# Kernel tuning notes

Hardware: AMD Instinct MI355X
Metric: run time of the kernel (lower is better)

Reference implementation:

```python
import jax, jax.numpy as jnp
import numpy as np

SC, ST, B, D, H, E, F, TOPK = 2048, 2048, 4, 256, 4, 8, 1024, 2
AUXW = 0.01
EPS = 1e-5


def setup_inputs() -> dict:
    key = jax.random.key(0)
    ks = jax.random.split(key, 16)
    s = 0.02
    n = lambda k, shp: (jax.random.normal(k, shp, jnp.float32) * s)
    z = lambda shp: jnp.zeros(shp, jnp.float32)
    o = lambda shp: jnp.ones(shp, jnp.float32)
    return {
        "x_context": jax.random.normal(ks[0], (SC, B, D), jnp.float32),
        "x_target": jax.random.normal(ks[1], (ST, B, D), jnp.float32),
        # shared self/cross attention (separate_att=False)
        "Wq": n(ks[2], (D, D)), "Wk": n(ks[3], (D, D)), "Wv": n(ks[4], (D, D)),
        "bq": z(D), "bk": z(D), "bv": z(D),
        "Wo": n(ks[5], (D, D)), "bo": z(D),
        # MoE gating + stacked 2-layer expert MLPs (D -> F -> D)
        "Wg": n(ks[6], (D, E)), "bg": z(E),
        "W1": n(ks[7], (E, D, F)), "b1": z((E, F)),
        "W2": n(ks[8], (E, F, D)), "b2": z((E, D)),
        # four post-LayerNorms
        "g_c1": o(D), "b_c1": z(D), "g_c2": o(D), "b_c2": z(D),
        "g_t1": o(D), "b_t1": z(D), "g_t2": o(D), "b_t2": z(D),
    }


def _ln(x, g, b):
    mu = x.mean(-1, keepdims=True)
    var = ((x - mu) ** 2).mean(-1, keepdims=True)
    return (x - mu) * jax.lax.rsqrt(var + EPS) * g + b


def _mha(q_in, kv, Wq, Wk, Wv, bq, bk, bv, Wo, bo):
    Sq, Bt, Dm = q_in.shape
    Sk = kv.shape[0]
    dh = Dm // H
    q = (q_in @ Wq + bq).reshape(Sq, Bt, H, dh)
    k = (kv @ Wk + bk).reshape(Sk, Bt, H, dh)
    v = (kv @ Wv + bv).reshape(Sk, Bt, H, dh)
    scores = jnp.einsum('qbhd,kbhd->bhqk', q, k) / jnp.asarray(np.sqrt(dh), q.dtype)
    attn = jax.nn.softmax(scores, axis=-1)
    out = jnp.einsum('bhqk,kbhd->qbhd', attn, v).reshape(Sq, Bt, Dm)
    return out @ Wo + bo


def _moe(x, Wg, bg, W1, b1, W2, b2):
    shp = x.shape
    xf = x.reshape(-1, shp[-1])          # [T, D]
    T = xf.shape[0]
    probs = jax.nn.softmax(xf @ Wg + bg, axis=-1)   # [T, E]
    gv, gi = jax.lax.top_k(probs, TOPK)
    gv = gv / gv.sum(-1, keepdims=True)
    # dense combine weights: gate value if expert selected else 0
    comb = jnp.zeros((T, E), xf.dtype).at[jnp.arange(T)[:, None], gi].add(gv)
    out = jnp.zeros_like(xf)
    for e in range(E):                    # fixed small expert loop
        h = jax.nn.relu(xf @ W1[e] + b1[e])
        out = out + (h @ W2[e] + b2[e]) * comb[:, e:e + 1]
    counts = probs.sum(0)
    frac = counts / counts.sum()
    aux = E * jnp.sum(frac * probs.mean(0))
    return out.reshape(shp), aux


def reference(x_context, x_target, Wq, Wk, Wv, bq, bk, bv, Wo, bo,
              Wg, bg, W1, b1, W2, b2,
              g_c1, b_c1, g_c2, b_c2, g_t1, b_t1, g_t2, b_t2):
    # context self-attention (post-norm)
    a = _mha(x_context, x_context, Wq, Wk, Wv, bq, bk, bv, Wo, bo)
    xc = _ln(a + x_context, g_c1, b_c1)
    f, aux1 = _moe(xc, Wg, bg, W1, b1, W2, b2)
    xc = _ln(f + xc, g_c2, b_c2)
    # target cross-attention over context (shared attention weights)
    a = _mha(x_target, xc, Wq, Wk, Wv, bq, bk, bv, Wo, bo)
    xt = _ln(a + x_target, g_t1, b_t1)
    f, aux2 = _moe(xt, Wg, bg, W1, b1, W2, b2)
    xt = _ln(f + xt, g_t2, b_t2)
    aux = AUXW * (aux1 + aux2)
    return xc, xt, aux
```

## Files before the change

kernel.cpp:

```cpp
#include <hip/hip_runtime.h>
#include <hip/hip_bf16.h>

typedef _Float16 f16_t;
typedef _Float16 f16x4v __attribute__((ext_vector_type(4)));
typedef _Float16 f16x8 __attribute__((ext_vector_type(8)));
typedef float f32x4 __attribute__((ext_vector_type(4)));

template<bool BIAS, bool OUTF16>
__global__ __launch_bounds__(256) void gemm16_kernel(
    const f16_t* __restrict__ A, const f16_t* __restrict__ B, void* __restrict__ Cv,
    const float* __restrict__ bias, int M, int N, int K, int lda, int ldb, int ldc)
{
    __shared__ f16_t As[64][72];
    __shared__ f16_t Bs[64][72];
    const int m0 = blockIdx.y * 64, n0 = blockIdx.x * 64;
    const int t = threadIdx.x, wave = t >> 6, lane = t & 63;
    const int wr = (wave >> 1) * 32, wc = (wave & 1) * 32;
    const int lr = lane & 15, kg = lane >> 4;
    const int sr = t >> 2, sc = (t & 3) * 16;
    const f16_t* arp = A + (long long)(m0 + sr) * lda;
    const f16_t* brp = B + (long long)(n0 + sr) * ldb;

    f32x4 acc[2][2] = {};
    for (int k0 = 0; k0 < K; k0 += 64) {
        *reinterpret_cast<f16x8*>(&As[sr][sc])     = *reinterpret_cast<const f16x8*>(&arp[k0 + sc]);
        *reinterpret_cast<f16x8*>(&As[sr][sc + 8]) = *reinterpret_cast<const f16x8*>(&arp[k0 + sc + 8]);
        *reinterpret_cast<f16x8*>(&Bs[sr][sc])     = *reinterpret_cast<const f16x8*>(&brp[k0 + sc]);
        *reinterpret_cast<f16x8*>(&Bs[sr][sc + 8]) = *reinterpret_cast<const f16x8*>(&brp[k0 + sc + 8]);
        __syncthreads();
        #pragma unroll
        for (int c = 0; c < 2; c++) {
            f16x8 a0 = *reinterpret_cast<const f16x8*>(&As[wr + lr][c * 32 + kg * 8]);
            f16x8 a1 = *reinterpret_cast<const f16x8*>(&As[wr + 16 + lr][c * 32 + kg * 8]);
            f16x8 b0 = *reinterpret_cast<const f16x8*>(&Bs[wc + lr][c * 32 + kg * 8]);
            f16x8 b1 = *reinterpret_cast<const f16x8*>(&Bs[wc + 16 + lr][c * 32 + kg * 8]);
            acc[0][0] = __builtin_amdgcn_mfma_f32_16x16x32_f16(a0, b0, acc[0][0], 0, 0, 0);
            acc[0][1] = __builtin_amdgcn_mfma_f32_16x16x32_f16(a0, b1, acc[0][1], 0, 0, 0);
            acc[1][0] = __builtin_amdgcn_mfma_f32_16x16x32_f16(a1, b0, acc[1][0], 0, 0, 0);
            acc[1][1] = __builtin_amdgcn_mfma_f32_16x16x32_f16(a1, b1, acc[1][1], 0, 0, 0);
        }
        __syncthreads();
    }
    #pragma unroll
    for (int mi = 0; mi < 2; mi++)
        #pragma unroll
        for (int ni = 0; ni < 2; ni++)
            #pragma unroll
            for (int r = 0; r < 4; r++) {
                const int row = m0 + wr + mi * 16 + kg * 4 + r;
                const int col = n0 + wc + ni * 16 + lr;
                float v = acc[mi][ni][r];
                if constexpr (BIAS) v += bias[col];
                if constexpr (OUTF16) ((f16_t*)Cv)[(long long)row * ldc + col] = (f16_t)v;
                else                  ((float*)Cv)[(long long)row * ldc + col] = v;
            }
}

__global__ __launch_bounds__(256) void qkv_kernel(
    const f16_t* __restrict__ Aq, const f16_t* __restrict__ Akv,
    const f16_t* __restrict__ B0, const f16_t* __restrict__ B1, const f16_t* __restrict__ B2,
    const float* __restrict__ bi0, const float* __restrict__ bi1, const float* __restrict__ bi2,
    f16_t* __restrict__ C0, f16_t* __restrict__ C1, f16_t* __restrict__ C2)
{
    const int zz = blockIdx.z;
    const f16_t* A = (zz == 0) ? Aq : Akv;
    const f16_t* B = (zz == 0) ? B0 : (zz == 1 ? B1 : B2);
    const float* bias = (zz == 0) ? bi0 : (zz == 1 ? bi1 : bi2);
    f16_t* C = (zz == 0) ? C0 : (zz == 1 ? C1 : C2);

    __shared__ f16_t As[64][72];
    __shared__ f16_t Bs[64][72];
    const int m0 = blockIdx.y * 64, n0 = blockIdx.x * 64;
    const int t = threadIdx.x, wave = t >> 6, lane = t & 63;
    const int wr = (wave >> 1) * 32, wc = (wave & 1) * 32;
    const int lr = lane & 15, kg = lane >> 4;
    const int sr = t >> 2, sc = (t & 3) * 16;
    const f16_t* arp = A + (long long)(m0 + sr) * 256;
    const f16_t* brp = B + (long long)(n0 + sr) * 256;

    f32x4 acc[2][2] = {};
    for (int k0 = 0; k0 < 256; k0 += 64) {
        *reinterpret_cast<f16x8*>(&As[sr][sc])     = *reinterpret_cast<const f16x8*>(&arp[k0 + sc]);
        *reinterpret_cast<f16x8*>(&As[sr][sc + 8]) = *reinterpret_cast<const f16x8*>(&arp[k0 + sc + 8]);
        *reinterpret_cast<f16x8*>(&Bs[sr][sc])     = *reinterpret_cast<const f16x8*>(&brp[k0 + sc]);
        *reinterpret_cast<f16x8*>(&Bs[sr][sc + 8]) = *reinterpret_cast<const f16x8*>(&brp[k0 + sc + 8]);
        __syncthreads();
        #pragma unroll
        for (int c = 0; c < 2; c++) {
            f16x8 a0 = *reinterpret_cast<const f16x8*>(&As[wr + lr][c * 32 + kg * 8]);
            f16x8 a1 = *reinterpret_cast<const f16x8*>(&As[wr + 16 + lr][c * 32 + kg * 8]);
            f16x8 b0 = *reinterpret_cast<const f16x8*>(&Bs[wc + lr][c * 32 + kg * 8]);
            f16x8 b1 = *reinterpret_cast<const f16x8*>(&Bs[wc + 16 + lr][c * 32 + kg * 8]);
            acc[0][0] = __builtin_amdgcn_mfma_f32_16x16x32_f16(a0, b0, acc[0][0], 0, 0, 0);
            acc[0][1] = __builtin_amdgcn_mfma_f32_16x16x32_f16(a0, b1, acc[0][1], 0, 0, 0);
            acc[1][0] = __builtin_amdgcn_mfma_f32_16x16x32_f16(a1, b0, acc[1][0], 0, 0, 0);
            acc[1][1] = __builtin_amdgcn_mfma_f32_16x16x32_f16(a1, b1, acc[1][1], 0, 0, 0);
        }
        __syncthreads();
    }
    #pragma unroll
    for (int mi = 0; mi < 2; mi++)
        #pragma unroll
        for (int ni = 0; ni < 2; ni++)
            #pragma unroll
            for (int r = 0; r < 4; r++) {
                const int row = m0 + wr + mi * 16 + kg * 4 + r;
                const int col = n0 + wc + ni * 16 + lr;
                C[(long long)row * 256 + col] = (f16_t)(acc[mi][ni][r] + bias[col]);
            }
}

template<bool GATHER, bool RELU, bool OUTF16>
__global__ __launch_bounds__(256) void moe_gemm16_kernel(
    const f16_t* __restrict__ A, const int* __restrict__ tok_of_slot,
    const f16_t* __restrict__ W, const float* __restrict__ bias,
    void* __restrict__ Cv, const int* __restrict__ ebase,
    int N, int K, int lda, int ldb, int ldc, int wstride, int bstride)
{
    const int m0 = blockIdx.y * 64;
    if (m0 >= ebase[8]) return;
    int e = 0;
    #pragma unroll
    for (int i = 1; i < 8; i++) if (m0 >= ebase[i]) e = i;
    const f16_t* __restrict__ B = W + (long long)e * wstride;
    const float* __restrict__ bs = bias + e * bstride;

    __shared__ f16_t As[64][72];
    __shared__ f16_t Bs[64][72];
    const int n0 = blockIdx.x * 64;
    const int t = threadIdx.x, wave = t >> 6, lane = t & 63;
    const int wr = (wave >> 1) * 32, wc = (wave & 1) * 32;
    const int lr = lane & 15, kg = lane >> 4;
    const int sr = t >> 2, sc = (t & 3) * 16;
    const f16_t* arp;
    if constexpr (GATHER) arp = A + (long long)(tok_of_slot[m0 + sr] & 8191) * lda;
    else                  arp = A + (long long)(m0 + sr) * lda;
    const f16_t* brp = B + (long long)(n0 + sr) * ldb;

    f32x4 acc[2][2] = {};
    for (int k0 = 0; k0 < K; k0 += 64) {
        *reinterpret_cast<f16x8*>(&As[sr][sc])     = *reinterpret_cast<const f16x8*>(&arp[k0 + sc]);
        *reinterpret_cast<f16x8*>(&As[sr][sc + 8]) = *reinterpret_cast<const f16x8*>(&arp[k0 + sc + 8]);
        *reinterpret_cast<f16x8*>(&Bs[sr][sc])     = *reinterpret_cast<const f16x8*>(&brp[k0 + sc]);
        *reinterpret_cast<f16x8*>(&Bs[sr][sc + 8]) = *reinterpret_cast<const f16x8*>(&brp[k0 + sc + 8]);
        __syncthreads();
        #pragma unroll
        for (int c = 0; c < 2; c++) {
            f16x8 a0 = *reinterpret_cast<const f16x8*>(&As[wr + lr][c * 32 + kg * 8]);
            f16x8 a1 = *reinterpret_cast<const f16x8*>(&As[wr + 16 + lr][c * 32 + kg * 8]);
            f16x8 b0 = *reinterpret_cast<const f16x8*>(&Bs[wc + lr][c * 32 + kg * 8]);
            f16x8 b1 = *reinterpret_cast<const f16x8*>(&Bs[wc + 16 + lr][c * 32 + kg * 8]);
            acc[0][0] = __builtin_amdgcn_mfma_f32_16x16x32_f16(a0, b0, acc[0][0], 0, 0, 0);
            acc[0][1] = __builtin_amdgcn_mfma_f32_16x16x32_f16(a0, b1, acc[0][1], 0, 0, 0);
            acc[1][0] = __builtin_amdgcn_mfma_f32_16x16x32_f16(a1, b0, acc[1][0], 0, 0, 0);
            acc[1][1] = __builtin_amdgcn_mfma_f32_16x16x32_f16(a1, b1, acc[1][1], 0, 0, 0);
        }
        __syncthreads();
    }
    #pragma unroll
    for (int mi = 0; mi < 2; mi++)
        #pragma unroll
        for (int ni = 0; ni < 2; ni++)
            #pragma unroll
            for (int r = 0; r < 4; r++) {
                const int row = m0 + wr + mi * 16 + kg * 4 + r;
                const int col = n0 + wc + ni * 16 + lr;
                float v = acc[mi][ni][r] + bs[col];
                if constexpr (RELU) v = fmaxf(v, 0.f);
                if constexpr (OUTF16) ((f16_t*)Cv)[(long long)row * ldc + col] = (f16_t)v;
                else                  ((float*)Cv)[(long long)row * ldc + col] = v;
            }
}

__global__ __launch_bounds__(256) void vtrans_kernel(
    const f16_t* __restrict__ V16, f16_t* __restrict__ VT)
{
    __shared__ f16_t tile[32][33];
    const int z = blockIdx.z;
    const int s0 = blockIdx.x * 32, d0 = blockIdx.y * 32;
    const int tx = threadIdx.x & 31, ty = threadIdx.x >> 5;
    #pragma unroll
    for (int i = 0; i < 32; i += 8)
        tile[ty + i][tx] = V16[(long long)(s0 + ty + i) * 1024 + 64 * z + d0 + tx];
    __syncthreads();
    #pragma unroll
    for (int i = 0; i < 32; i += 8)
        VT[(long long)z * 131072 + (long long)(d0 + ty + i) * 2048 + s0 + tx] = tile[tx][ty + i];
}

__global__ __launch_bounds__(256, 6) void flash_kernel(
    const f16_t* __restrict__ Q16, const f16_t* __restrict__ K16,
    const f16_t* __restrict__ VT, f16_t* __restrict__ Opart,
    float* __restrict__ mlm, float* __restrict__ mll)
{
    __shared__ f16_t KVs[64][72];
    __shared__ f16_t Ps[4][16][72];

    const int z = blockIdx.y;
    const int c = blockIdx.z;
    const int m0 = blockIdx.x * 64;
    const int t = threadIdx.x, w = t >> 6, lane = t & 63;
    const int lr = lane & 15, kg = lane >> 4;
    const long long cbase = 64LL * z;

    f16x8 qf0, qf1;
    {
        const long long qrow = (long long)(m0 + w * 16 + lr) * 1024 + cbase;
        qf0 = *reinterpret_cast<const f16x8*>(&Q16[qrow + kg * 8]);
        qf1 = *reinterpret_cast<const f16x8*>(&Q16[qrow + 32 + kg * 8]);
        #pragma unroll
        for (int i = 0; i < 8; i++) { qf0[i] *= (f16_t)0.125f; qf1[i] *= (f16_t)0.125f; }
    }

    f32x4 oacc[4] = {};
    float mrun[4] = { -1e30f, -1e30f, -1e30f, -1e30f };
    float lrun[4] = {};

    const int sr = t >> 2, sc = (t & 3) * 16;
    const int nbeg = c * 512;
    for (int n0 = nbeg; n0 < nbeg + 512; n0 += 64) {
        const long long krow = (long long)(n0 + sr) * 1024 + cbase;
        *reinterpret_cast<f16x8*>(&KVs[sr][sc])     = *reinterpret_cast<const f16x8*>(&K16[krow + sc]);
        *reinterpret_cast<f16x8*>(&KVs[sr][sc + 8]) = *reinterpret_cast<const f16x8*>(&K16[krow + sc + 8]);
        __syncthreads();

        float sv[4][4];
        #pragma unroll
        for (int nt = 0; nt < 4; nt++) {
            f32x4 acc = {};
            f16x8 b0 = *reinterpret_cast<const f16x8*>(&KVs[nt * 16 + lr][kg * 8]);
            f16x8 b1 = *reinterpret_cast<const f16x8*>(&KVs[nt * 16 + lr][32 + kg * 8]);
            acc = __builtin_amdgcn_mfma_f32_16x16x32_f16(qf0, b0, acc, 0, 0, 0);
            acc = __builtin_amdgcn_mfma_f32_16x16x32_f16(qf1, b1, acc, 0, 0, 0);
            #pragma unroll
            for (int r = 0; r < 4; r++) sv[nt][r] = acc[r];
        }

        float mnew[4], alpha[4];
        #pragma unroll
        for (int r = 0; r < 4; r++) {
            float rm = fmaxf(fmaxf(sv[0][r], sv[1][r]), fmaxf(sv[2][r], sv[3][r]));
            rm = fmaxf(rm, __shfl_xor(rm, 1));
            rm = fmaxf(rm, __shfl_xor(rm, 2));
            rm = fmaxf(rm, __shfl_xor(rm, 4));
            rm = fmaxf(rm, __shfl_xor(rm, 8));
            mnew[r] = fmaxf(mrun[r], rm);
            alpha[r] = __expf(mrun[r] - mnew[r]);
            mrun[r] = mnew[r];
        }
        #pragma unroll
        for (int nt = 0; nt < 4; nt++)
            #pragma unroll
            for (int r = 0; r < 4; r++) sv[nt][r] = __expf(sv[nt][r] - mnew[r]);
        #pragma unroll
        for (int r = 0; r < 4; r++) {
            float rs = sv[0][r] + sv[1][r] + sv[2][r] + sv[3][r];
            rs += __shfl_xor(rs, 1);
            rs += __shfl_xor(rs, 2);
            rs += __shfl_xor(rs, 4);
            rs += __shfl_xor(rs, 8);
            lrun[r] = lrun[r] * alpha[r] + rs;
        }
        #pragma unroll
        for (int dt = 0; dt < 4; dt++)
            #pragma unroll
            for (int r = 0; r < 4; r++) oacc[dt][r] *= alpha[r];

        #pragma unroll
        for (int nt = 0; nt < 4; nt++)
            #pragma unroll
            for (int r = 0; r < 4; r++)
                Ps[w][kg * 4 + r][nt * 16 + lr] = (f16_t)sv[nt][r];

        __syncthreads();

        const long long vrow = (long long)z * 131072 + (long long)sr * 2048 + n0;
        *reinterpret_cast<f16x8*>(&KVs[sr][sc])     = *reinterpret_cast<const f16x8*>(&VT[vrow + sc]);
        *reinterpret_cast<f16x8*>(&KVs[sr][sc + 8]) = *reinterpret_cast<const f16x8*>(&VT[vrow + sc + 8]);
        __syncthreads();

        f16x8 pa0 = *reinterpret_cast<const f16x8*>(&Ps[w][lr][kg * 8]);
        f16x8 pa1 = *reinterpret_cast<const f16x8*>(&Ps[w][lr][32 + kg * 8]);
        #pragma unroll
        for (int dt = 0; dt < 4; dt++) {
            f16x8 vb0 = *reinterpret_cast<const f16x8*>(&KVs[dt * 16 + lr][kg * 8]);
            f16x8 vb1 = *reinterpret_cast<const f16x8*>(&KVs[dt * 16 + lr][32 + kg * 8]);
            oacc[dt] = __builtin_amdgcn_mfma_f32_16x16x32_f16(pa0, vb0, oacc[dt], 0, 0, 0);
            oacc[dt] = __builtin_amdgcn_mfma_f32_16x16x32_f16(pa1, vb1, oacc[dt], 0, 0, 0);
        }
        __syncthreads();
    }

    f16_t* op = Opart + (long long)c * 2097152;
    const long long orow0 = (long long)(m0 + w * 16) * 1024 + cbase;
    #pragma unroll
    for (int r = 0; r < 4; r++)
        #pragma unroll
        for (int dt = 0; dt < 4; dt++)
            op[orow0 + (long long)(kg * 4 + r) * 1024 + dt * 16 + lr] = (f16_t)oacc[dt][r];
    if (lr == 0) {
        const int b = z >> 2, h = z & 3;
        #pragma unroll
        for (int r = 0; r < 4; r++) {
            const int tok = (m0 + w * 16 + kg * 4 + r) * 4 + b;
            const long long idx = (long long)(c * 4 + h) * 8192 + tok;
            mlm[idx] = mrun[r];
            mll[idx] = lrun[r];
        }
    }
}

__global__ __launch_bounds__(256) void merge_kernel(
    const f16_t* __restrict__ Opart, const float* __restrict__ mlm,
    const float* __restrict__ mll, f16_t* __restrict__ O16)
{
    const int w = threadIdx.x >> 6, lane = threadIdx.x & 63;
    const int trow = blockIdx.x * 4 + w;
    const int h = lane >> 4;
    float m[4], l[4];
    #pragma unroll
    for (int c = 0; c < 4; c++) {
        m[c] = mlm[(long long)(c * 4 + h) * 8192 + trow];
        l[c] = mll[(long long)(c * 4 + h) * 8192 + trow];
    }
    float M = fmaxf(fmaxf(m[0], m[1]), fmaxf(m[2], m[3]));
    float wv[4], L = 0.f;
    #pragma unroll
    for (int c = 0; c < 4; c++) { wv[c] = __expf(m[c] - M); L += wv[c] * l[c]; }
    const float inv = 1.f / L;
    const long long base = (long long)trow * 256 + lane * 4;
    float acc[4] = {};
    #pragma unroll
    for (int c = 0; c < 4; c++) {
        f16x4v v = *reinterpret_cast<const f16x4v*>(&Opart[(long long)c * 2097152 + base]);
        #pragma unroll
        for (int j = 0; j < 4; j++) acc[j] += wv[c] * (float)v[j];
    }
    f16_t o[4] = { (f16_t)(acc[0] * inv), (f16_t)(acc[1] * inv),
                   (f16_t)(acc[2] * inv), (f16_t)(acc[3] * inv) };
    *reinterpret_cast<ulong1*>(&O16[base]) = *reinterpret_cast<ulong1*>(o);
}

__global__ __launch_bounds__(256) void wtrans_kernel(
    const float* __restrict__ in, f16_t* __restrict__ out, int R, int C)
{
    __shared__ float tile[32][33];
    const long long zoff = (long long)blockIdx.z * R * C;
    const int r0 = blockIdx.y * 32, c0 = blockIdx.x * 32;
    const int tx = threadIdx.x & 31, ty = threadIdx.x >> 5;
    #pragma unroll
    for (int i = 0; i < 32; i += 8)
        tile[ty + i][tx] = in[zoff + (long long)(r0 + ty + i) * C + c0 + tx];
    __syncthreads();
    #pragma unroll
    for (int i = 0; i < 32; i += 8)
        out[zoff + (long long)(c0 + ty + i) * R + r0 + tx] = (f16_t)tile[tx][ty + i];
}

__global__ __launch_bounds__(256) void wtrans4_kernel(
    const float* __restrict__ W0, const float* __restrict__ W1,
    const float* __restrict__ W2, const float* __restrict__ W3,
    f16_t* __restrict__ T0, f16_t* __restrict__ T1,
    f16_t* __restrict__ T2, f16_t* __restrict__ T3)
{
    __shared__ float tile[32][33];
    const int z = blockIdx.z;
    const float* in = (z == 0) ? W0 : (z == 1 ? W1 : (z == 2 ? W2 : W3));
    f16_t* out = (z == 0) ? T0 : (z == 1 ? T1 : (z == 2 ? T2 : T3));
    const int r0 = blockIdx.y * 32, c0 = blockIdx.x * 32;
    const int tx = threadIdx.x & 31, ty = threadIdx.x >> 5;
    #pragma unroll
    for (int i = 0; i < 32; i += 8)
        tile[ty + i][tx] = in[(long long)(r0 + ty + i) * 256 + c0 + tx];
    __syncthreads();
    #pragma unroll
    for (int i = 0; i < 32; i += 8)
        out[(long long)(c0 + ty + i) * 256 + r0 + tx] = (f16_t)tile[tx][ty + i];
}

__global__ __launch_bounds__(256) void cvt16_kernel(
    const float* __restrict__ a, const float* __restrict__ b,
    f16_t* __restrict__ oa, f16_t* __restrict__ ob)
{
    long long i = ((long long)blockIdx.x * 256 + threadIdx.x) * 4;
    const float* in = a; f16_t* out = oa;
    if (i >= 2097152) { in = b; out = ob; i -= 2097152; }
    float4 v = *reinterpret_cast<const float4*>(&in[i]);
    f16_t o[4] = { (f16_t)v.x, (f16_t)v.y, (f16_t)v.z, (f16_t)v.w };
    *reinterpret_cast<ulong1*>(&out[i]) = *reinterpret_cast<ulong1*>(o);
}

__global__ __launch_bounds__(256) void ln_kernel(
    const float* __restrict__ in1, const float* __restrict__ in2,
    const float* __restrict__ gamma, const float* __restrict__ beta,
    float* __restrict__ out, f16_t* __restrict__ out16)
{
    const int wave = threadIdx.x >> 6, lane = threadIdx.x & 63;
    const long long row = (long long)blockIdx.x * 4 + wave;
    const long long base = row * 256 + lane * 4;
    float4 a = *reinterpret_cast<const float4*>(&in1[base]);
    float4 b = *reinterpret_cast<const float4*>(&in2[base]);
    float x[4] = { a.x + b.x, a.y + b.y, a.z + b.z, a.w + b.w };
    float s = x[0] + x[1] + x[2] + x[3];
    float s2 = x[0]*x[0] + x[1]*x[1] + x[2]*x[2] + x[3]*x[3];
    #pragma unroll
    for (int o = 32; o; o >>= 1) { s += __shfl_xor(s, o); s2 += __shfl_xor(s2, o); }
    const float mean = s * (1.f / 256.f);
    const float var = s2 * (1.f / 256.f) - mean * mean;
    const float rstd = rsqrtf(var + 1e-5f);
    float4 g = *reinterpret_cast<const float4*>(&gamma[lane * 4]);
    float4 bb = *reinterpret_cast<const float4*>(&beta[lane * 4]);
    const float* gf = reinterpret_cast<const float*>(&g);
    const float* bf = reinterpret_cast<const float*>(&bb);
    float y[4];
    #pragma unroll
    for (int i = 0; i < 4; i++) y[i] = (x[i] - mean) * rstd * gf[i] + bf[i];
    *reinterpret_cast<float4*>(&out[base]) = make_float4(y[0], y[1], y[2], y[3]);
    if (out16) {
        f16_t o[4] = { (f16_t)y[0], (f16_t)y[1], (f16_t)y[2], (f16_t)y[3] };
        *reinterpret_cast<ulong1*>(&out16[base]) = *reinterpret_cast<ulong1*>(o);
    }
}

__global__ __launch_bounds__(256) void gating_kernel(
    const float* __restrict__ X, const float* __restrict__ Wg, const float* __restrict__ bg,
    int* __restrict__ gcount, float* __restrict__ counts,
    int* __restrict__ pos_of_tok, int* __restrict__ exp_of_tok,
    float* __restrict__ gate_of_tok)
{
    __shared__ float WgL[2048];
    __shared__ float cpart[8];
    __shared__ int lcnt[8];
    __shared__ int lbase[8];
    const int t = threadIdx.x;
    for (int i = t; i < 2048; i += 256) WgL[i] = Wg[i];
    if (t < 8) { cpart[t] = 0.f; lcnt[t] = 0; }
    __syncthreads();

    const int tok = blockIdx.x * 256 + t;
    const float* xr = X + (long long)tok * 256;
    float acc[8] = {};
    for (int k = 0; k < 256; k += 4) {
        float4 xv = *reinterpret_cast<const float4*>(xr + k);
        const float* xf = reinterpret_cast<const float*>(&xv);
        #pragma unroll
        for (int i = 0; i < 4; i++) {
            const float xi = xf[i];
            const float* wrow = &WgL[(k + i) * 8];
            #pragma unroll
            for (int e = 0; e < 8; e++) acc[e] += xi * wrow[e];
        }
    }
    float p[8]; float mx = -1e30f;
    #pragma unroll
    for (int e = 0; e < 8; e++) { p[e] = acc[e] + bg[e]; mx = fmaxf(mx, p[e]); }
    float se = 0.f;
    #pragma unroll
    for (int e = 0; e < 8; e++) { p[e] = __expf(p[e] - mx); se += p[e]; }
    const float inv = 1.f / se;
    #pragma unroll
    for (int e = 0; e < 8; e++) { p[e] *= inv; atomicAdd(&cpart[e], p[e]); }

    int i1 = 0;
    #pragma unroll
    for (int e = 1; e < 8; e++) if (p[e] > p[i1]) i1 = e;
    int i2 = (i1 == 0) ? 1 : 0;
    #pragma unroll
    for (int e = 0; e < 8; e++) if (e != i1 && p[e] > p[i2]) i2 = e;
    const float gs = 1.f / (p[i1] + p[i2]);

    const int p1 = atomicAdd(&lcnt[i1], 1);
    const int p2 = atomicAdd(&lcnt[i2], 1);
    __syncthreads();
    if (t < 8) {
        lbase[t] = atomicAdd(&gcount[t], lcnt[t]);
        atomicAdd(&counts[t], cpart[t]);
    }
    __syncthreads();
    pos_of_tok[2 * tok]     = lbase[i1] + p1;
    pos_of_tok[2 * tok + 1] = lbase[i2] + p2;
    exp_of_tok[2 * tok]     = i1;
    exp_of_tok[2 * tok + 1] = i2;
    gate_of_tok[2 * tok]     = p[i1] * gs;
    gate_of_tok[2 * tok + 1] = p[i2] * gs;
}

__global__ void finalize_kernel(const int* __restrict__ gcount, int* __restrict__ ebase)
{
    if (threadIdx.x == 0) {
        int b = 0;
        for (int e = 0; e < 8; e++) { ebase[e] = b; b += (gcount[e] + 63) & ~63; }
        ebase[8] = b;
    }
}

__global__ __launch_bounds__(256) void scatter_kernel(
    const int* __restrict__ pos_of_tok, const int* __restrict__ exp_of_tok,
    const int* __restrict__ ebase, int* __restrict__ tok_of_slot)
{
    const int i = blockIdx.x * 256 + threadIdx.x;
    const int e = exp_of_tok[i];
    tok_of_slot[ebase[e] + pos_of_tok[i]] = i >> 1;
}

__global__ __launch_bounds__(256) void moe_combine_ln_kernel(
    const float* __restrict__ Ys, const float* __restrict__ X1,
    const int* __restrict__ pos_of_tok, const int* __restrict__ exp_of_tok,
    const float* __restrict__ gate_of_tok, const int* __restrict__ ebase,
    const float* __restrict__ gamma, const float* __restrict__ beta,
    float* __restrict__ out, f16_t* __restrict__ out16)
{
    const int wave = threadIdx.x >> 6, lane = threadIdx.x & 63;
    const long long tok = (long long)blockIdx.x * 4 + wave;
    const int e1 = exp_of_tok[2 * tok], e2 = exp_of_tok[2 * tok + 1];
    const long long s1 = ebase[e1] + pos_of_tok[2 * tok];
    const long long s2 = ebase[e2] + pos_of_tok[2 * tok + 1];
    const float gv1 = gate_of_tok[2 * tok], gv2 = gate_of_tok[2 * tok + 1];
    const long long base = tok * 256 + lane * 4;
    float4 y1 = *reinterpret_cast<const float4*>(&Ys[s1 * 256 + lane * 4]);
    float4 y2 = *reinterpret_cast<const float4*>(&Ys[s2 * 256 + lane * 4]);
    float4 xv = *reinterpret_cast<const float4*>(&X1[base]);
    float x[4] = { gv1 * y1.x + gv2 * y2.x + xv.x,
                   gv1 * y1.y + gv2 * y2.y + xv.y,
                   gv1 * y1.z + gv2 * y2.z + xv.z,
                   gv1 * y1.w + gv2 * y2.w + xv.w };
    float s = x[0] + x[1] + x[2] + x[3];
    float s2v = x[0]*x[0] + x[1]*x[1] + x[2]*x[2] + x[3]*x[3];
    #pragma unroll
    for (int o = 32; o; o >>= 1) { s += __shfl_xor(s, o); s2v += __shfl_xor(s2v, o); }
    const float mean = s * (1.f / 256.f);
    const float var = s2v * (1.f / 256.f) - mean * mean;
    const float rstd = rsqrtf(var + 1e-5f);
    float4 g = *reinterpret_cast<const float4*>(&gamma[lane * 4]);
    float4 bb = *reinterpret_cast<const float4*>(&beta[lane * 4]);
    const float* gf = reinterpret_cast<const float*>(&g);
    const float* bf = reinterpret_cast<const float*>(&bb);
    float y[4];
    #pragma unroll
    for (int i = 0; i < 4; i++) y[i] = (x[i] - mean) * rstd * gf[i] + bf[i];
    *reinterpret_cast<float4*>(&out[base]) = make_float4(y[0], y[1], y[2], y[3]);
    if (out16) {
        f16_t o[4] = { (f16_t)y[0], (f16_t)y[1], (f16_t)y[2], (f16_t)y[3] };
        *reinterpret_cast<ulong1*>(&out16[base]) = *reinterpret_cast<ulong1*>(o);
    }
}

__global__ void aux_kernel(const float* __restrict__ counts, float* __restrict__ out)
{
    if (threadIdx.x == 0) {
        float aux = 0.f;
        for (int pzz = 0; pzz < 2; pzz++) {
            const float* c = counts + pzz * 8;
            float tot = 0.f;
            for (int e = 0; e < 8; e++) tot += c[e];
            float s = 0.f;
            for (int e = 0; e < 8; e++) s += (c[e] / tot) * (c[e] * (1.f / 8192.f));
            aux += 8.f * s;
        }
        out[0] = 0.01f * aux;
    }
}

extern "C" void kernel_launch(void* const* d_in, const int* in_sizes, int n_in,
                              void* d_out, int out_size, void* d_ws, size_t ws_size,
                              hipStream_t stream)
{
    const float* Xc  = (const float*)d_in[0];
    const float* Xt  = (const float*)d_in[1];
    const float* Wq  = (const float*)d_in[2];
    const float* Wk  = (const float*)d_in[3];
    const float* Wv  = (const float*)d_in[4];
    const float* bq  = (const float*)d_in[5];
    const float* bk  = (const float*)d_in[6];
    const float* bv  = (const float*)d_in[7];
    const float* Wo  = (const float*)d_in[8];
    const float* bo  = (const float*)d_in[9];
    const float* Wg  = (const float*)d_in[10];
    const float* bg  = (const float*)d_in[11];
    const float* W1  = (const float*)d_in[12];
    const float* b1  = (const float*)d_in[13];
    const float* W2  = (const float*)d_in[14];
    const float* b2  = (const float*)d_in[15];
    const float* g_c1 = (const float*)d_in[16];
    const float* b_c1 = (const float*)d_in[17];
    const float* g_c2 = (const float*)d_in[18];
    const float* b_c2 = (const float*)d_in[19];
    const float* g_t1 = (const float*)d_in[20];
    const float* b_t1 = (const float*)d_in[21];
    const float* g_t2 = (const float*)d_in[22];
    const float* b_t2 = (const float*)d_in[23];

    const long long NTOK = 2097152;
    const int SLOT_MAX = 16896;
    float* dout = (float*)d_out;
    float* xcout = dout;
    float* xtout = dout + NTOK;

    float* ws = (float*)d_ws;
    float* P1 = ws;
    float* X1 = P1 + NTOK;
    float* Ys = X1 + NTOK;
    float* counts      = Ys + (long long)SLOT_MAX * 256;
    int*   gcount      = (int*)(counts + 16);
    float* gate_of_tok = (float*)(gcount + 16);
    float* mlm = gate_of_tok + 16384;
    float* mll = mlm + 131072;
    int* ebase       = (int*)(mll + 131072);
    int* pos_of_tok  = ebase + 16;
    int* exp_of_tok  = pos_of_tok + 16384;
    int* tok_of_slot = exp_of_tok + 16384;
    f16_t* h16 = (f16_t*)(tok_of_slot + SLOT_MAX);
    f16_t* Xc16 = h16;
    f16_t* Xt16 = Xc16 + NTOK;
    f16_t* xc16 = Xt16 + NTOK;
    f16_t* Q16  = xc16 + NTOK;
    f16_t* K16  = Q16 + NTOK;
    f16_t* V16  = K16 + NTOK;
    f16_t* O16  = V16 + NTOK;
    f16_t* X116 = O16 + NTOK;
    f16_t* VT   = X116 + NTOK;
    f16_t* Hs16 = VT + NTOK;
    f16_t* WqT  = Hs16 + (long long)SLOT_MAX * 1024;
    f16_t* WkT  = WqT + 65536;
    f16_t* WvT  = WkT + 65536;
    f16_t* WoT  = WvT + 65536;
    f16_t* W1T  = WoT + 65536;
    f16_t* W2T  = W1T + 2097152;
    f16_t* Opart = Hs16;

    hipMemsetAsync(counts, 0, 32 * sizeof(int), stream);

    cvt16_kernel<<<4096, 256, 0, stream>>>(Xc, Xt, Xc16, Xt16);
    wtrans4_kernel<<<dim3(8, 8, 4), 256, 0, stream>>>(Wq, Wk, Wv, Wo, WqT, WkT, WvT, WoT);
    wtrans_kernel<<<dim3(32, 8, 8), 256, 0, stream>>>(W1, W1T, 256, 1024);
    wtrans_kernel<<<dim3(8, 32, 8), 256, 0, stream>>>(W2, W2T, 1024, 256);

    for (int pass = 0; pass < 2; pass++) {
        const float*  xq    = pass ? Xt   : Xc;
        const f16_t*  xq16  = pass ? Xt16 : Xc16;
        const f16_t*  xkv16 = pass ? xc16 : Xc16;
        const float* g1  = pass ? g_t1 : g_c1;
        const float* be1 = pass ? b_t1 : b_c1;
        const float* g2  = pass ? g_t2 : g_c2;
        const float* be2 = pass ? b_t2 : b_c2;
        float* cnt = counts + pass * 8;
        int* gcnt  = gcount + pass * 8;
        float* oln = pass ? xtout : xcout;
        f16_t* oln16 = pass ? nullptr : xc16;

        qkv_kernel<<<dim3(4, 128, 3), 256, 0, stream>>>(
            xq16, xkv16, WqT, WkT, WvT, bq, bk, bv, Q16, K16, V16);

        vtrans_kernel<<<dim3(64, 2, 16), 256, 0, stream>>>(V16, VT);
        flash_kernel<<<dim3(32, 16, 4), 256, 0, stream>>>(Q16, K16, VT, Opart, mlm, mll);
        merge_kernel<<<2048, 256, 0, stream>>>(Opart, mlm, mll, O16);

        gemm16_kernel<true,false><<<dim3(4, 128), 256, 0, stream>>>(
            O16, WoT, P1, bo, 8192, 256, 256, 256, 256, 256);
        ln_kernel<<<2048, 256, 0, stream>>>(P1, xq, g1, be1, X1, X116);

        gating_kernel<<<32, 256, 0, stream>>>(X1, Wg, bg, gcnt, cnt,
                                              pos_of_tok, exp_of_tok, gate_of_tok);
        finalize_kernel<<<1, 64, 0, stream>>>(gcnt, ebase);
        scatter_kernel<<<64, 256, 0, stream>>>(pos_of_tok, exp_of_tok, ebase, tok_of_slot);
        moe_gemm16_kernel<true,true,true><<<dim3(16, 264), 256, 0, stream>>>(
            X116, tok_of_slot, W1T, b1, Hs16, ebase,
            1024, 256, 256, 256, 1024, 262144, 1024);
        moe_gemm16_kernel<false,false,false><<<dim3(4, 264), 256, 0, stream>>>(
            Hs16, nullptr, W2T, b2, Ys, ebase,
            256, 1024, 1024, 1024, 256, 262144, 256);
        moe_combine_ln_kernel<<<2048, 256, 0, stream>>>(
            Ys, X1, pos_of_tok, exp_of_tok, gate_of_tok, ebase, g2, be2, oln, oln16);
    }

    aux_kernel<<<1, 64, 0, stream>>>(counts, dout + 2 * NTOK);
}
```

Baseline: 580.9 us.

## Use 128x128 GEMM tiles, prefetch K/V in flash, store MoE output as fp16

All GEMMs (QKV, output projection, both MoE expert GEMMs) now go through one shared body that computes 128x128 tiles, each wave holding a 4x4 set of MFMA accumulators. Expert padding is changed to 128 rows to match. The aim is more reuse of data staged in shared memory and fewer global loads per FLOP, at the cost of more registers, lower occupancy, fewer blocks and more padding waste. The flash kernel now loads the next K/V tile into registers before computing on the current one, and the second MoE GEMM writes fp16 instead of fp32, halving that traffic at some precision cost.

```diff
diff --git a/kernel.cpp b/kernel.cpp
--- a/kernel.cpp
+++ b/kernel.cpp
@@ -6,57 +6,77 @@
 typedef _Float16 f16x8 __attribute__((ext_vector_type(8)));
 typedef float f32x4 __attribute__((ext_vector_type(4)));
 
-template<bool BIAS, bool OUTF16>
-__global__ __launch_bounds__(256) void gemm16_kernel(
-    const f16_t* __restrict__ A, const f16_t* __restrict__ B, void* __restrict__ Cv,
-    const float* __restrict__ bias, int M, int N, int K, int lda, int ldb, int ldc)
-{
-    __shared__ f16_t As[64][72];
-    __shared__ f16_t Bs[64][72];
-    const int m0 = blockIdx.y * 64, n0 = blockIdx.x * 64;
+template<bool BIAS, bool RELU, bool OUTF16, bool GATHER>
+__device__ __forceinline__ void gemm128_body(
+    const f16_t* __restrict__ A, const f16_t* __restrict__ B,
+    void* __restrict__ Cv, const float* __restrict__ bias,
+    const int* __restrict__ tok_of_slot,
+    int m0, int n0, int K, int lda, int ldb, int ldc)
+{
+    __shared__ f16_t As[128][72];
+    __shared__ f16_t Bs[128][72];
     const int t = threadIdx.x, wave = t >> 6, lane = t & 63;
-    const int wr = (wave >> 1) * 32, wc = (wave & 1) * 32;
+    const int wr2 = (wave >> 1) * 64, wc2 = (wave & 1) * 64;
     const int lr = lane & 15, kg = lane >> 4;
-    const int sr = t >> 2, sc = (t & 3) * 16;
-    const f16_t* arp = A + (long long)(m0 + sr) * lda;
+    const int sr = t >> 1, sc0 = (t & 1) * 32;
+
+    const f16_t* arp;
+    if constexpr (GATHER) arp = A + (long long)(tok_of_slot[m0 + sr] & 8191) * lda;
+    else                  arp = A + (long long)(m0 + sr) * lda;
     const f16_t* brp = B + (long long)(n0 + sr) * ldb;
 
-    f32x4 acc[2][2] = {};
+    f32x4 acc[4][4] = {};
     for (int k0 = 0; k0 < K; k0 += 64) {
-        *reinterpret_cast<f16x8*>(&As[sr][sc])     = *reinterpret_cast<const f16x8*>(&arp[k0 + sc]);
-        *reinterpret_cast<f16x8*>(&As[sr][sc + 8]) = *reinterpret_cast<const f16x8*>(&arp[k0 + sc + 8]);
-        *reinterpret_cast<f16x8*>(&Bs[sr][sc])     = *reinterpret_cast<const f16x8*>(&brp[k0 + sc]);
-        *reinterpret_cast<f16x8*>(&Bs[sr][sc + 8]) = *reinterpret_cast<const f16x8*>(&brp[k0 + sc + 8]);
+        #pragma unroll
+        for (int j = 0; j < 4; j++) {
+            *reinterpret_cast<f16x8*>(&As[sr][sc0 + j * 8]) =
+                *reinterpret_cast<const f16x8*>(&arp[k0 + sc0 + j * 8]);
+            *reinterpret_cast<f16x8*>(&Bs[sr][sc0 + j * 8]) =
+                *reinterpret_cast<const f16x8*>(&brp[k0 + sc0 + j * 8]);
+        }
         __syncthreads();
         #pragma unroll
         for (int c = 0; c < 2; c++) {
-            f16x8 a0 = *reinterpret_cast<const f16x8*>(&As[wr + lr][c * 32 + kg * 8]);
-            f16x8 a1 = *reinterpret_cast<const f16x8*>(&As[wr + 16 + lr][c * 32 + kg * 8]);
-            f16x8 b0 = *reinterpret_cast<const f16x8*>(&Bs[wc + lr][c * 32 + kg * 8]);
-            f16x8 b1 = *reinterpret_cast<const f16x8*>(&Bs[wc + 16 + lr][c * 32 + kg * 8]);
-            acc[0][0] = __builtin_amdgcn_mfma_f32_16x16x32_f16(a0, b0, acc[0][0], 0, 0, 0);
-            acc[0][1] = __builtin_amdgcn_mfma_f32_16x16x32_f16(a0, b1, acc[0][1], 0, 0, 0);
-            acc[1][0] = __builtin_amdgcn_mfma_f32_16x16x32_f16(a1, b0, acc[1][0], 0, 0, 0);
-            acc[1][1] = __builtin_amdgcn_mfma_f32_16x16x32_f16(a1, b1, acc[1][1], 0, 0, 0);
+            f16x8 av[4], bv[4];
+            #pragma unroll
+            for (int i = 0; i < 4; i++) {
+                av[i] = *reinterpret_cast<const f16x8*>(&As[wr2 + i * 16 + lr][c * 32 + kg * 8]);
+                bv[i] = *reinterpret_cast<const f16x8*>(&Bs[wc2 + i * 16 + lr][c * 32 + kg * 8]);
+            }
+            #pragma unroll
+            for (int mi = 0; mi < 4; mi++)
+                #pragma unroll
+                for (int ni = 0; ni < 4; ni++)
+                    acc[mi][ni] = __builtin_amdgcn_mfma_f32_16x16x32_f16(av[mi], bv[ni], acc[mi][ni], 0, 0, 0);
         }
         __syncthreads();
     }
     #pragma unroll
-    for (int mi = 0; mi < 2; mi++)
-        #pragma unroll
-        for (int ni = 0; ni < 2; ni++)
+    for (int mi = 0; mi < 4; mi++)
+        #pragma unroll
+        for (int ni = 0; ni < 4; ni++)
             #pragma unroll
             for (int r = 0; r < 4; r++) {
-                const int row = m0 + wr + mi * 16 + kg * 4 + r;
-                const int col = n0 + wc + ni * 16 + lr;
+                const int row = m0 + wr2 + mi * 16 + kg * 4 + r;
+                const int col = n0 + wc2 + ni * 16 + lr;
                 float v = acc[mi][ni][r];
                 if constexpr (BIAS) v += bias[col];
+                if constexpr (RELU) v = fmaxf(v, 0.f);
                 if constexpr (OUTF16) ((f16_t*)Cv)[(long long)row * ldc + col] = (f16_t)v;
                 else                  ((float*)Cv)[(long long)row * ldc + col] = v;
             }
 }
 
-__global__ __launch_bounds__(256) void qkv_kernel(
+template<bool BIAS, bool OUTF16>
+__global__ __launch_bounds__(256) void gemm128_kernel(
+    const f16_t* __restrict__ A, const f16_t* __restrict__ B, void* __restrict__ Cv,
+    const float* __restrict__ bias, int K, int lda, int ldb, int ldc)
+{
+    gemm128_body<BIAS, false, OUTF16, false>(A, B, Cv, bias, nullptr,
+                                             blockIdx.y * 128, blockIdx.x * 128, K, lda, ldb, ldc);
+}
+
+__global__ __launch_bounds__(256) void qkv128_kernel(
     const f16_t* __restrict__ Aq, const f16_t* __restrict__ Akv,
     const f16_t* __restrict__ B0, const f16_t* __restrict__ B1, const f16_t* __restrict__ B2,
     const float* __restrict__ bi0, const float* __restrict__ bi1, const float* __restrict__ bi2,
@@ -67,109 +87,25 @@
     const f16_t* B = (zz == 0) ? B0 : (zz == 1 ? B1 : B2);
     const float* bias = (zz == 0) ? bi0 : (zz == 1 ? bi1 : bi2);
     f16_t* C = (zz == 0) ? C0 : (zz == 1 ? C1 : C2);
-
-    __shared__ f16_t As[64][72];
-    __shared__ f16_t Bs[64][72];
-    const int m0 = blockIdx.y * 64, n0 = blockIdx.x * 64;
-    const int t = threadIdx.x, wave = t >> 6, lane = t & 63;
-    const int wr = (wave >> 1) * 32, wc = (wave & 1) * 32;
-    const int lr = lane & 15, kg = lane >> 4;
-    const int sr = t >> 2, sc = (t & 3) * 16;
-    const f16_t* arp = A + (long long)(m0 + sr) * 256;
-    const f16_t* brp = B + (long long)(n0 + sr) * 256;
-
-    f32x4 acc[2][2] = {};
-    for (int k0 = 0; k0 < 256; k0 += 64) {
-        *reinterpret_cast<f16x8*>(&As[sr][sc])     = *reinterpret_cast<const f16x8*>(&arp[k0 + sc]);
-        *reinterpret_cast<f16x8*>(&As[sr][sc + 8]) = *reinterpret_cast<const f16x8*>(&arp[k0 + sc + 8]);
-        *reinterpret_cast<f16x8*>(&Bs[sr][sc])     = *reinterpret_cast<const f16x8*>(&brp[k0 + sc]);
-        *reinterpret_cast<f16x8*>(&Bs[sr][sc + 8]) = *reinterpret_cast<const f16x8*>(&brp[k0 + sc + 8]);
-        __syncthreads();
-        #pragma unroll
-        for (int c = 0; c < 2; c++) {
-            f16x8 a0 = *reinterpret_cast<const f16x8*>(&As[wr + lr][c * 32 + kg * 8]);
-            f16x8 a1 = *reinterpret_cast<const f16x8*>(&As[wr + 16 + lr][c * 32 + kg * 8]);
-            f16x8 b0 = *reinterpret_cast<const f16x8*>(&Bs[wc + lr][c * 32 + kg * 8]);
-            f16x8 b1 = *reinterpret_cast<const f16x8*>(&Bs[wc + 16 + lr][c * 32 + kg * 8]);
-            acc[0][0] = __builtin_amdgcn_mfma_f32_16x16x32_f16(a0, b0, acc[0][0], 0, 0, 0);
-            acc[0][1] = __builtin_amdgcn_mfma_f32_16x16x32_f16(a0, b1, acc[0][1], 0, 0, 0);
-            acc[1][0] = __builtin_amdgcn_mfma_f32_16x16x32_f16(a1, b0, acc[1][0], 0, 0, 0);
-            acc[1][1] = __builtin_amdgcn_mfma_f32_16x16x32_f16(a1, b1, acc[1][1], 0, 0, 0);
-        }
-        __syncthreads();
-    }
-    #pragma unroll
-    for (int mi = 0; mi < 2; mi++)
-        #pragma unroll
-        for (int ni = 0; ni < 2; ni++)
-            #pragma unroll
-            for (int r = 0; r < 4; r++) {
-                const int row = m0 + wr + mi * 16 + kg * 4 + r;
-                const int col = n0 + wc + ni * 16 + lr;
-                C[(long long)row * 256 + col] = (f16_t)(acc[mi][ni][r] + bias[col]);
-            }
-}
-
-template<bool GATHER, bool RELU, bool OUTF16>
-__global__ __launch_bounds__(256) void moe_gemm16_kernel(
+    gemm128_body<true, false, true, false>(A, B, C, bias, nullptr,
+                                           blockIdx.y * 128, blockIdx.x * 128, 256, 256, 256, 256);
+}
+
+template<bool RELU, bool OUTF16, bool GATHER>
+__global__ __launch_bounds__(256) void moe_gemm128_kernel(
     const f16_t* __restrict__ A, const int* __restrict__ tok_of_slot,
     const f16_t* __restrict__ W, const float* __restrict__ bias,
     void* __restrict__ Cv, const int* __restrict__ ebase,
-    int N, int K, int lda, int ldb, int ldc, int wstride, int bstride)
-{
-    const int m0 = blockIdx.y * 64;
+    int K, int lda, int ldb, int ldc, int wstride, int bstride)
+{
+    const int m0 = blockIdx.y * 128;
     if (m0 >= ebase[8]) return;
     int e = 0;
     #pragma unroll
     for (int i = 1; i < 8; i++) if (m0 >= ebase[i]) e = i;
-    const f16_t* __restrict__ B = W + (long long)e * wstride;
-    const float* __restrict__ bs = bias + e * bstride;
-
-    __shared__ f16_t As[64][72];
-    __shared__ f16_t Bs[64][72];
-    const int n0 = blockIdx.x * 64;
-    const int t = threadIdx.x, wave = t >> 6, lane = t & 63;
-    const int wr = (wave >> 1) * 32, wc = (wave & 1) * 32;
-    const int lr = lane & 15, kg = lane >> 4;
-    const int sr = t >> 2, sc = (t & 3) * 16;
-    const f16_t* arp;
-    if constexpr (GATHER) arp = A + (long long)(tok_of_slot[m0 + sr] & 8191) * lda;
-    else                  arp = A + (long long)(m0 + sr) * lda;
-    const f16_t* brp = B + (long long)(n0 + sr) * ldb;
-
-    f32x4 acc[2][2] = {};
-    for (int k0 = 0; k0 < K; k0 += 64) {
-        *reinterpret_cast<f16x8*>(&As[sr][sc])     = *reinterpret_cast<const f16x8*>(&arp[k0 + sc]);
-        *reinterpret_cast<f16x8*>(&As[sr][sc + 8]) = *reinterpret_cast<const f16x8*>(&arp[k0 + sc + 8]);
-        *reinterpret_cast<f16x8*>(&Bs[sr][sc])     = *reinterpret_cast<const f16x8*>(&brp[k0 + sc]);
-        *reinterpret_cast<f16x8*>(&Bs[sr][sc + 8]) = *reinterpret_cast<const f16x8*>(&brp[k0 + sc + 8]);
-        __syncthreads();
-        #pragma unroll
-        for (int c = 0; c < 2; c++) {
-            f16x8 a0 = *reinterpret_cast<const f16x8*>(&As[wr + lr][c * 32 + kg * 8]);
-            f16x8 a1 = *reinterpret_cast<const f16x8*>(&As[wr + 16 + lr][c * 32 + kg * 8]);
-            f16x8 b0 = *reinterpret_cast<const f16x8*>(&Bs[wc + lr][c * 32 + kg * 8]);
-            f16x8 b1 = *reinterpret_cast<const f16x8*>(&Bs[wc + 16 + lr][c * 32 + kg * 8]);
-            acc[0][0] = __builtin_amdgcn_mfma_f32_16x16x32_f16(a0, b0, acc[0][0], 0, 0, 0);
-            acc[0][1] = __builtin_amdgcn_mfma_f32_16x16x32_f16(a0, b1, acc[0][1], 0, 0, 0);
-            acc[1][0] = __builtin_amdgcn_mfma_f32_16x16x32_f16(a1, b0, acc[1][0], 0, 0, 0);
-            acc[1][1] = __builtin_amdgcn_mfma_f32_16x16x32_f16(a1, b1, acc[1][1], 0, 0, 0);
-        }
-        __syncthreads();
-    }
-    #pragma unroll
-    for (int mi = 0; mi < 2; mi++)
-        #pragma unroll
-        for (int ni = 0; ni < 2; ni++)
-            #pragma unroll
-            for (int r = 0; r < 4; r++) {
-                const int row = m0 + wr + mi * 16 + kg * 4 + r;
-                const int col = n0 + wc + ni * 16 + lr;
-                float v = acc[mi][ni][r] + bs[col];
-                if constexpr (RELU) v = fmaxf(v, 0.f);
-                if constexpr (OUTF16) ((f16_t*)Cv)[(long long)row * ldc + col] = (f16_t)v;
-                else                  ((float*)Cv)[(long long)row * ldc + col] = v;
-            }
+    gemm128_body<true, RELU, OUTF16, GATHER>(
+        A, W + (long long)e * wstride, Cv, bias + e * bstride, tok_of_slot,
+        m0, blockIdx.x * 128, K, lda, ldb, ldc);
 }
 
 __global__ __launch_bounds__(256) void vtrans_kernel(
@@ -217,12 +153,27 @@
     float lrun[4] = {};
 
     const int sr = t >> 2, sc = (t & 3) * 16;
-    const int nbeg = c * 512;
-    for (int n0 = nbeg; n0 < nbeg + 512; n0 += 64) {
-        const long long krow = (long long)(n0 + sr) * 1024 + cbase;
-        *reinterpret_cast<f16x8*>(&KVs[sr][sc])     = *reinterpret_cast<const f16x8*>(&K16[krow + sc]);
-        *reinterpret_cast<f16x8*>(&KVs[sr][sc + 8]) = *reinterpret_cast<const f16x8*>(&K16[krow + sc + 8]);
+    const int nbeg = c * 512, nend = nbeg + 512;
+
+    f16x8 ka, kb, va, vb;
+    {
+        const long long krow = (long long)(nbeg + sr) * 1024 + cbase;
+        ka = *reinterpret_cast<const f16x8*>(&K16[krow + sc]);
+        kb = *reinterpret_cast<const f16x8*>(&K16[krow + sc + 8]);
+        const long long vrow = (long long)z * 131072 + (long long)sr * 2048 + nbeg;
+        va = *reinterpret_cast<const f16x8*>(&VT[vrow + sc]);
+        vb = *reinterpret_cast<const f16x8*>(&VT[vrow + sc + 8]);
+    }
+
+    for (int n0 = nbeg; n0 < nend; n0 += 64) {
+        *reinterpret_cast<f16x8*>(&KVs[sr][sc])     = ka;
+        *reinterpret_cast<f16x8*>(&KVs[sr][sc + 8]) = kb;
         __syncthreads();
+        if (n0 + 64 < nend) {
+            const long long krow = (long long)(n0 + 64 + sr) * 1024 + cbase;
+            ka = *reinterpret_cast<const f16x8*>(&K16[krow + sc]);
+            kb = *reinterpret_cast<const f16x8*>(&K16[krow + sc + 8]);
+        }
 
         float sv[4][4];
         #pragma unroll
@@ -274,10 +225,14 @@
 
         __syncthreads();
 
-        const long long vrow = (long long)z * 131072 + (long long)sr * 2048 + n0;
-        *reinterpret_cast<f16x8*>(&KVs[sr][sc])     = *reinterpret_cast<const f16x8*>(&VT[vrow + sc]);
-        *reinterpret_cast<f16x8*>(&KVs[sr][sc + 8]) = *reinterpret_cast<const f16x8*>(&VT[vrow + sc + 8]);
+        *reinterpret_cast<f16x8*>(&KVs[sr][sc])     = va;
+        *reinterpret_cast<f16x8*>(&KVs[sr][sc + 8]) = vb;
         __syncthreads();
+        if (n0 + 64 < nend) {
+            const long long vrow = (long long)z * 131072 + (long long)sr * 2048 + (n0 + 64);
+            va = *reinterpret_cast<const f16x8*>(&VT[vrow + sc]);
+            vb = *reinterpret_cast<const f16x8*>(&VT[vrow + sc + 8]);
+        }
 
         f16x8 pa0 = *reinterpret_cast<const f16x8*>(&Ps[w][lr][kg * 8]);
         f16x8 pa1 = *reinterpret_cast<const f16x8*>(&Ps[w][lr][32 + kg * 8]);
@@ -489,7 +444,7 @@
 {
     if (threadIdx.x == 0) {
         int b = 0;
-        for (int e = 0; e < 8; e++) { ebase[e] = b; b += (gcount[e] + 63) & ~63; }
+        for (int e = 0; e < 8; e++) { ebase[e] = b; b += (gcount[e] + 127) & ~127; }
         ebase[8] = b;
     }
 }
@@ -504,7 +459,7 @@
 }
 
 __global__ __launch_bounds__(256) void moe_combine_ln_kernel(
-    const float* __restrict__ Ys, const float* __restrict__ X1,
+    const f16_t* __restrict__ Ys, const float* __restrict__ X1,
     const int* __restrict__ pos_of_tok, const int* __restrict__ exp_of_tok,
     const float* __restrict__ gate_of_tok, const int* __restrict__ ebase,
     const float* __restrict__ gamma, const float* __restrict__ beta,
@@ -517,13 +472,13 @@
     const long long s2 = ebase[e2] + pos_of_tok[2 * tok + 1];
     const float gv1 = gate_of_tok[2 * tok], gv2 = gate_of_tok[2 * tok + 1];
     const long long base = tok * 256 + lane * 4;
-    float4 y1 = *reinterpret_cast<const float4*>(&Ys[s1 * 256 + lane * 4]);
-    float4 y2 = *reinterpret_cast<const float4*>(&Ys[s2 * 256 + lane * 4]);
+    f16x4v y1 = *reinterpret_cast<const f16x4v*>(&Ys[s1 * 256 + lane * 4]);
+    f16x4v y2 = *reinterpret_cast<const f16x4v*>(&Ys[s2 * 256 + lane * 4]);
     float4 xv = *reinterpret_cast<const float4*>(&X1[base]);
-    float x[4] = { gv1 * y1.x + gv2 * y2.x + xv.x,
-                   gv1 * y1.y + gv2 * y2.y + xv.y,
-                   gv1 * y1.z + gv2 * y2.z + xv.z,
-                   gv1 * y1.w + gv2 * y2.w + xv.w };
+    const float* xf = reinterpret_cast<const float*>(&xv);
+    float x[4];
+    #pragma unroll
+    for (int i = 0; i < 4; i++) x[i] = gv1 * (float)y1[i] + gv2 * (float)y2[i] + xf[i];
     float s = x[0] + x[1] + x[2] + x[3];
     float s2v = x[0]*x[0] + x[1]*x[1] + x[2]*x[2] + x[3]*x[3];
     #pragma unroll
@@ -591,7 +546,7 @@
     const float* b_t2 = (const float*)d_in[23];
 
     const long long NTOK = 2097152;
-    const int SLOT_MAX = 16896;
+    const int SLOT_MAX = 17408;
     float* dout = (float*)d_out;
     float* xcout = dout;
     float* xtout = dout + NTOK;
@@ -599,8 +554,7 @@
     float* ws = (float*)d_ws;
     float* P1 = ws;
     float* X1 = P1 + NTOK;
-    float* Ys = X1 + NTOK;
-    float* counts      = Ys + (long long)SLOT_MAX * 256;
+    float* counts      = X1 + NTOK;
     int*   gcount      = (int*)(counts + 16);
     float* gate_of_tok = (float*)(gcount + 16);
     float* mlm = gate_of_tok + 16384;
@@ -620,7 +574,8 @@
     f16_t* X116 = O16 + NTOK;
     f16_t* VT   = X116 + NTOK;
     f16_t* Hs16 = VT + NTOK;
-    f16_t* WqT  = Hs16 + (long long)SLOT_MAX * 1024;
+    f16_t* Ys16 = Hs16 + (long long)SLOT_MAX * 1024;
+    f16_t* WqT  = Ys16 + (long long)SLOT_MAX * 256;
     f16_t* WkT  = WqT + 65536;
     f16_t* WvT  = WkT + 65536;
     f16_t* WoT  = WvT + 65536;
@@ -648,29 +603,29 @@
         float* oln = pass ? xtout : xcout;
         f16_t* oln16 = pass ? nullptr : xc16;
 
-        qkv_kernel<<<dim3(4, 128, 3), 256, 0, stream>>>(
+        qkv128_kernel<<<dim3(2, 64, 3), 256, 0, stream>>>(
             xq16, xkv16, WqT, WkT, WvT, bq, bk, bv, Q16, K16, V16);
 
         vtrans_kernel<<<dim3(64, 2, 16), 256, 0, stream>>>(V16, VT);
         flash_kernel<<<dim3(32, 16, 4), 256, 0, stream>>>(Q16, K16, VT, Opart, mlm, mll);
         merge_kernel<<<2048, 256, 0, stream>>>(Opart, mlm, mll, O16);
 
-        gemm16_kernel<true,false><<<dim3(4, 128), 256, 0, stream>>>(
-            O16, WoT, P1, bo, 8192, 256, 256, 256, 256, 256);
+        gemm128_kernel<true, false><<<dim3(2, 64), 256, 0, stream>>>(
+            O16, WoT, P1, bo, 256, 256, 256, 256);
         ln_kernel<<<2048, 256, 0, stream>>>(P1, xq, g1, be1, X1, X116);
 
         gating_kernel<<<32, 256, 0, stream>>>(X1, Wg, bg, gcnt, cnt,
                                               pos_of_tok, exp_of_tok, gate_of_tok);
         finalize_kernel<<<1, 64, 0, stream>>>(gcnt, ebase);
         scatter_kernel<<<64, 256, 0, stream>>>(pos_of_tok, exp_of_tok, ebase, tok_of_slot);
-        moe_gemm16_kernel<true,true,true><<<dim3(16, 264), 256, 0, stream>>>(
+        moe_gemm128_kernel<true, true, true><<<dim3(8, 136), 256, 0, stream>>>(
             X116, tok_of_slot, W1T, b1, Hs16, ebase,
-            1024, 256, 256, 256, 1024, 262144, 1024);
-        moe_gemm16_kernel<false,false,false><<<dim3(4, 264), 256, 0, stream>>>(
-            Hs16, nullptr, W2T, b2, Ys, ebase,
-            256, 1024, 1024, 1024, 256, 262144, 256);
+            256, 256, 256, 1024, 262144, 1024);
+        moe_gemm128_kernel<false, true, false><<<dim3(2, 136), 256, 0, stream>>>(
+            Hs16, nullptr, W2T, b2, Ys16, ebase,
+            1024, 1024, 1024, 256, 262144, 256);
         moe_combine_ln_kernel<<<2048, 256, 0, stream>>>(
-            Ys, X1, pos_of_tok, exp_of_tok, gate_of_tok, ebase, g2, be2, oln, oln16);
+            Ys16, X1, pos_of_tok, exp_of_tok, gate_of_tok, ebase, g2, be2, oln, oln16);
     }
 
     aux_kernel<<<1, 64, 0, stream>>>(counts, dout + 2 * NTOK);
```

Measured after the change: 592.3 us. Within noise of the previous version (+2.0%).
